# Kernel tuning notes

Hardware: AMD Instinct MI355X
Metric: run time of the kernel (lower is better)

The kernel has to match this reference:

```python
import jax, jax.numpy as jnp
import numpy as np

R_EARTH_KM = 6371.0

def haversine(lat1, lon1, lat2, lon2):
    # inputs in degrees, output distance in km
    lat1, lon1, lat2, lon2 = (jnp.radians(x) for x in (lat1, lon1, lat2, lon2))
    dlat = lat2 - lat1
    dlon = lon2 - lon1
    a = jnp.sin(dlat * 0.5) ** 2 + jnp.cos(lat1) * jnp.cos(lat2) * jnp.sin(dlon * 0.5) ** 2
    return 2.0 * R_EARTH_KM * jnp.arcsin(jnp.sqrt(jnp.clip(a, 0.0, 1.0)))

def _latlon(key, n):
    k1, k2 = jax.random.split(key)
    lat = jax.random.uniform(k1, (n,), minval=-90.0, maxval=90.0)
    lon = jax.random.uniform(k2, (n,), minval=-180.0, maxval=180.0)
    return jnp.stack([lat, lon], axis=1).astype(jnp.float32)

def setup_inputs() -> dict:
    key = jax.random.key(0)
    ks = jax.random.split(key, 12)
    B, D = 4096, 1792
    NC, NM, NF = 3000, 7000, 13000
    scale = 0.02
    return {
        'features': jax.random.normal(ks[0], (B, D), dtype=jnp.float32),
        'labels_2d': _latlon(ks[1], B),
        'coarse_partition': _latlon(ks[2], NC),
        'middle_partition': _latlon(ks[3], NM),
        'fine_partition': _latlon(ks[4], NF),
        'middle_parents': jax.random.randint(ks[5], (NM,), 0, NC, dtype=jnp.int32),
        'fine_parents': jax.random.randint(ks[6], (NF,), 0, NM, dtype=jnp.int32),
        'coarse_w': jax.random.normal(ks[7], (D, NC), dtype=jnp.float32) * scale,
        'coarse_b': jnp.zeros((NC,), dtype=jnp.float32),
        'middle_w': jax.random.normal(ks[8], (D, NM), dtype=jnp.float32) * scale,
        'middle_b': jnp.zeros((NM,), dtype=jnp.float32),
        'fine_w': jax.random.normal(ks[9], (D, NF), dtype=jnp.float32) * scale,
        'fine_b': jnp.zeros((NF,), dtype=jnp.float32),
    }

def _single_loss(labels_2d, logits, partition):
    # cartesian-product haversine cdist: [B, M]
    dists = haversine(labels_2d[:, 0:1], labels_2d[:, 1:2],
                      partition[None, :, 0], partition[None, :, 1])
    labels_index = jnp.argmin(dists, axis=1)
    logp = jax.nn.log_softmax(logits, axis=1)
    nll = -jnp.take_along_axis(logp, labels_index[:, None], axis=1)[:, 0]
    return jnp.mean(nll)

def reference(features, labels_2d, coarse_partition, middle_partition, fine_partition,
              middle_parents, fine_parents, coarse_w, coarse_b, middle_w, middle_b,
              fine_w, fine_b):
    coarse_logits = features @ coarse_w + coarse_b
    middle_logits = features @ middle_w + middle_b
    fine_logits = features @ fine_w + fine_b

    loss = (_single_loss(labels_2d, coarse_logits, coarse_partition)
            + _single_loss(labels_2d, middle_logits, middle_partition)
            + _single_loss(labels_2d, fine_logits, fine_partition))

    fine_probs = jax.nn.softmax(fine_logits, axis=1)
    middle_probs = jax.nn.softmax(middle_logits, axis=1)
    coarse_probs = jax.nn.softmax(coarse_logits, axis=1)
    # hierarchy combine: gather parent probs and multiply
    final_probs = (fine_probs
                   * middle_probs[:, fine_parents]
                   * coarse_probs[:, middle_parents[fine_parents]])

    predictions = fine_partition[jnp.argmax(final_probs, axis=1)]  # [B, 2]
    d = haversine(labels_2d[:, 0], labels_2d[:, 1], predictions[:, 0], predictions[:, 1])
    thresholds = jnp.array([1.0, 25.0, 200.0, 750.0, 2500.0], dtype=jnp.float32)
    acc = jnp.mean((d[None, :] <= thresholds[:, None]).astype(jnp.float32), axis=1)
    return loss, acc
```

## Files before the change

kernel.cpp:

```cpp
#include <hip/hip_runtime.h>
#include <hip/hip_fp16.h>
#include <math.h>

#define B_   4096
#define D_   1792
#define NC_  3000
#define NM_  7000
#define NF_  13000
#define NCP  3072
#define NMP  7040
#define NFP  13056
#define NTOT (NCP + NMP + NFP)
#define OFFC 0
#define OFFM NCP
#define OFFF (NCP + NMP)
#define FHALF 6528
#define WCHUNK 7040
#define DEG2RAD 0.017453292519943295f

typedef _Float16 half8  __attribute__((ext_vector_type(8)));
typedef _Float16 half4v __attribute__((ext_vector_type(4)));
typedef float    f32x4  __attribute__((ext_vector_type(4)));

__device__ __forceinline__ void async16(const void* g, void* l) {
  __builtin_amdgcn_global_load_lds(
      (const __attribute__((address_space(1))) void*)g,
      (__attribute__((address_space(3))) void*)l, 16, 0, 0);
}

__global__ void prep_kernel(const float* __restrict__ labels,
                            const float* __restrict__ cp, const float* __restrict__ mp,
                            const float* __restrict__ fp,
                            const float* __restrict__ cb, const float* __restrict__ mb,
                            const float* __restrict__ fb,
                            float* __restrict__ bias, float4* __restrict__ ptrig,
                            float4* __restrict__ ltrig, float* __restrict__ accum) {
  int i = blockIdx.x * 256 + threadIdx.x;
  if (i < NTOT) {
    float v = 0.f;
    if (i < OFFM)      { if (i < NC_) v = cb[i]; }
    else if (i < OFFF) { int j = i - OFFM; if (j < NM_) v = mb[j]; }
    else               { int j = i - OFFF; if (j < NF_) v = fb[j]; }
    bias[i] = v;
  }
  if (i < NC_ + NM_ + NF_) {
    const float* src; int j = i;
    if (i < NC_)            { src = cp; }
    else if (i < NC_ + NM_) { src = mp; j = i - NC_; }
    else                    { src = fp; j = i - NC_ - NM_; }
    float la = src[2 * j] * DEG2RAD, lo = src[2 * j + 1] * DEG2RAD;
    float sla, cla, slo, clo;
    sincosf(la, &sla, &cla); sincosf(lo, &slo, &clo);
    ptrig[i] = make_float4(sla, cla, slo, clo);
  }
  if (i < B_) {
    float la = labels[2 * i] * DEG2RAD, lo = labels[2 * i + 1] * DEG2RAD;
    float sla, cla, slo, clo;
    sincosf(la, &sla, &cla); sincosf(lo, &slo, &clo);
    ltrig[i] = make_float4(sla, cla, slo, clo);
  }
  if (i < 64) accum[i] = 0.f;
}

__global__ void cvt_feat(const float4* __restrict__ in, half4v* __restrict__ out) {
  int i = blockIdx.x * 256 + threadIdx.x;
  float4 v = in[i];
  half4v h;
  h[0] = (_Float16)v.x; h[1] = (_Float16)v.y; h[2] = (_Float16)v.z; h[3] = (_Float16)v.w;
  out[i] = h;
}

__global__ void transpose_w(const float* __restrict__ w, _Float16* __restrict__ wt,
                            int Nfull, int c0, int ntrue_chunk) {
  __shared__ float tile[32][33];
  int n0 = blockIdx.x * 32, k0 = blockIdx.y * 32;
  int tx = threadIdx.x, ty = threadIdx.y;
#pragma unroll
  for (int i = 0; i < 4; ++i) {
    int kk = ty + i * 8;
    int n = n0 + tx;
    float v = (n < ntrue_chunk) ? w[(size_t)(k0 + kk) * Nfull + c0 + n] : 0.f;
    tile[kk][tx] = v;
  }
  __syncthreads();
#pragma unroll
  for (int i = 0; i < 4; ++i) {
    int nn = ty + i * 8;
    wt[(size_t)(n0 + nn) * D_ + k0 + tx] = (_Float16)tile[tx][nn];
  }
}

__global__ void argmin_kernel(const float4* __restrict__ ptrig, const float4* __restrict__ ltrig,
                              int* __restrict__ lidx) {
  __shared__ float rv[256];
  __shared__ int ri[256];
  int b = blockIdx.x, tid = threadIdx.x;
  float4 lt = ltrig[b];
  const int base[3] = {0, NC_, NC_ + NM_};
  const int cnt[3]  = {NC_, NM_, NF_};
#pragma unroll
  for (int h = 0; h < 3; ++h) {
    float best = 1e30f; int bi = 0;
    for (int i = tid; i < cnt[h]; i += 256) {
      float4 pt = ptrig[base[h] + i];
      float cdla = lt.y * pt.y + lt.x * pt.x;
      float cdlo = lt.w * pt.w + lt.z * pt.z;
      float a = 0.5f * (1.f - cdla) + (lt.y * pt.y) * 0.5f * (1.f - cdlo);
      if (a < best) { best = a; bi = i; }
    }
    rv[tid] = best; ri[tid] = bi;
    __syncthreads();
    for (int o = 128; o; o >>= 1) {
      if (tid < o) {
        if (rv[tid + o] < rv[tid] || (rv[tid + o] == rv[tid] && ri[tid + o] < ri[tid])) {
          rv[tid] = rv[tid + o]; ri[tid] = ri[tid + o];
        }
      }
      __syncthreads();
    }
    if (tid == 0) lidx[h * B_ + b] = ri[0];
    __syncthreads();
  }
}

__global__ __launch_bounds__(256) void gemm_f16(const _Float16* __restrict__ A,
                                                const _Float16* __restrict__ Bt,
                                                const float* __restrict__ bias,
                                                _Float16* __restrict__ C, int coff) {
  __shared__ _Float16 tA[128 * 64];
  __shared__ _Float16 tB[128 * 64];
  const int tid = threadIdx.x;
  const int lane = tid & 63, w = tid >> 6;
  const int wm = w & 1, wn = w >> 1;
  const int q = lane >> 4, l15 = lane & 15;
  const int bx = blockIdx.x;
  const int mt = bx & 31, nt = bx >> 5;
  const int m0 = mt * 128;
  const int nl0 = nt * 128;
  const int gn0 = coff + nl0;

  f32x4 acc[4][4];
#pragma unroll
  for (int a = 0; a < 4; ++a)
#pragma unroll
    for (int b2 = 0; b2 < 4; ++b2) acc[a][b2] = (f32x4){0.f, 0.f, 0.f, 0.f};

  const int cbase = w * 256 + lane;
  int amoff[4], axor[4], bnoff[4], bxor[4];
#pragma unroll
  for (int t = 0; t < 4; ++t) {
    int ml = wm * 64 + t * 16 + l15;
    amoff[t] = ml * 64; axor[t] = ml & 7;
    int nl = wn * 64 + t * 16 + l15;
    bnoff[t] = nl * 64; bxor[t] = nl & 7;
  }

  for (int kt = 0; kt < 28; ++kt) {
    const int k0 = kt * 64;
#pragma unroll
    for (int t = 0; t < 4; ++t) {
      int c = cbase + t * 64;
      int m = c >> 3, slot = c & 7;
      int kb = slot ^ (m & 7);
      async16(A + (size_t)(m0 + m) * D_ + k0 + kb * 8, (void*)(tA + (w * 4 + t) * 512));
      async16(Bt + (size_t)(nl0 + m) * D_ + k0 + kb * 8, (void*)(tB + (w * 4 + t) * 512));
    }
    __syncthreads();
#pragma unroll
    for (int s = 0; s < 2; ++s) {
      half8 af[4], bf[4];
#pragma unroll
      for (int t = 0; t < 4; ++t) {
        af[t] = *(const half8*)(tA + amoff[t] + ((((s << 2) | q) ^ axor[t]) << 3));
        bf[t] = *(const half8*)(tB + bnoff[t] + ((((s << 2) | q) ^ bxor[t]) << 3));
      }
#pragma unroll
      for (int tm = 0; tm < 4; ++tm)
#pragma unroll
        for (int tn = 0; tn < 4; ++tn)
          acc[tm][tn] = __builtin_amdgcn_mfma_f32_16x16x32_f16(af[tm], bf[tn], acc[tm][tn], 0, 0, 0);
    }
    __syncthreads();
  }

  float bn[4];
#pragma unroll
  for (int tn = 0; tn < 4; ++tn) bn[tn] = bias[gn0 + wn * 64 + tn * 16 + l15];
#pragma unroll
  for (int tm = 0; tm < 4; ++tm) {
    int gm = m0 + wm * 64 + tm * 16 + q * 4;
#pragma unroll
    for (int tn = 0; tn < 4; ++tn) {
      int gn = gn0 + wn * 64 + tn * 16 + l15;
      _Float16* dst = C + (size_t)gm * NTOT + gn;
#pragma unroll
      for (int r = 0; r < 4; ++r) dst[(size_t)r * NTOT] = (_Float16)(acc[tm][tn][r] + bn[tn]);
    }
  }
}

__device__ __forceinline__ float block_lse(float m, float s, float* ms, float* ss, int tid) {
  ms[tid] = m; ss[tid] = s;
  __syncthreads();
  for (int o = 128; o; o >>= 1) {
    if (tid < o) {
      float m2 = ms[tid + o], s2 = ss[tid + o];
      if (m2 > ms[tid]) { ss[tid] = s2 + ss[tid] * __expf(ms[tid] - m2); ms[tid] = m2; }
      else ss[tid] += s2 * __expf(m2 - ms[tid]);
    }
    __syncthreads();
  }
  float r = ms[0] + logf(ss[0]);
  __syncthreads();
  return r;
}

__global__ __launch_bounds__(256) void final_kernel(const _Float16* __restrict__ logits,
                                                    const int* __restrict__ mpar,
                                                    const int* __restrict__ fpar,
                                                    const float4* __restrict__ ptrig,
                                                    const float4* __restrict__ ltrig,
                                                    const int* __restrict__ lidx,
                                                    float* __restrict__ nll_buf,
                                                    float* __restrict__ accum) {
  __shared__ float co[NC_];
  __shared__ float par[NM_];
  __shared__ float ms[256], ss[256];
  __shared__ int ri[256];
  int b = blockIdx.x, tid = threadIdx.x;
  const _Float16* row = logits + (size_t)b * NTOT;

  float m = -1e30f, s = 0.f;
  {
    const half8* rc = (const half8*)(row + OFFC);
    for (int i = tid; i < NC_ / 8; i += 256) {
      half8 v = rc[i];
      float x[8];
#pragma unroll
      for (int j = 0; j < 8; ++j) x[j] = (float)v[j];
      float vm = fmaxf(fmaxf(fmaxf(x[0], x[1]), fmaxf(x[2], x[3])),
                       fmaxf(fmaxf(x[4], x[5]), fmaxf(x[6], x[7])));
      if (vm > m) { s *= __expf(m - vm); m = vm; }
#pragma unroll
      for (int j = 0; j < 8; ++j) s += __expf(x[j] - m);
      f32x4 lo = {x[0], x[1], x[2], x[3]}, hi = {x[4], x[5], x[6], x[7]};
      *(f32x4*)(co + i * 8)     = lo;
      *(f32x4*)(co + i * 8 + 4) = hi;
    }
  }
  float lseC = block_lse(m, s, ms, ss, tid);

  m = -1e30f; s = 0.f;
  {
    const half8* rm = (const half8*)(row + OFFM);
    const int4* mp4 = (const int4*)mpar;
    for (int i = tid; i < NM_ / 8; i += 256) {
      half8 v = rm[i];
      int4 p0 = mp4[2 * i], p1 = mp4[2 * i + 1];
      float x[8];
#pragma unroll
      for (int j = 0; j < 8; ++j) x[j] = (float)v[j];
      float vm = fmaxf(fmaxf(fmaxf(x[0], x[1]), fmaxf(x[2], x[3])),
                       fmaxf(fmaxf(x[4], x[5]), fmaxf(x[6], x[7])));
      if (vm > m) { s *= __expf(m - vm); m = vm; }
#pragma unroll
      for (int j = 0; j < 8; ++j) s += __expf(x[j] - m);
      int pj[8] = {p0.x, p0.y, p0.z, p0.w, p1.x, p1.y, p1.z, p1.w};
      f32x4 lo = {x[0] + co[pj[0]], x[1] + co[pj[1]], x[2] + co[pj[2]], x[3] + co[pj[3]]};
      f32x4 hi = {x[4] + co[pj[4]], x[5] + co[pj[5]], x[6] + co[pj[6]], x[7] + co[pj[7]]};
      *(f32x4*)(par + i * 8)     = lo;
      *(f32x4*)(par + i * 8 + 4) = hi;
    }
  }
  float lseM = block_lse(m, s, ms, ss, tid);

  m = -1e30f; s = 0.f;
  float best = -1e30f; int bi = 0;
  {
    const half8* rf = (const half8*)(row + OFFF);
    const int4* fp4 = (const int4*)fpar;
    for (int i = tid; i < NF_ / 8; i += 256) {
      half8 v = rf[i];
      int4 p0 = fp4[2 * i], p1 = fp4[2 * i + 1];
      float x[8];
#pragma unroll
      for (int j = 0; j < 8; ++j) x[j] = (float)v[j];
      float vm = fmaxf(fmaxf(fmaxf(x[0], x[1]), fmaxf(x[2], x[3])),
                       fmaxf(fmaxf(x[4], x[5]), fmaxf(x[6], x[7])));
      if (vm > m) { s *= __expf(m - vm); m = vm; }
#pragma unroll
      for (int j = 0; j < 8; ++j) s += __expf(x[j] - m);
      int pj[8] = {p0.x, p0.y, p0.z, p0.w, p1.x, p1.y, p1.z, p1.w};
#pragma unroll
      for (int j = 0; j < 8; ++j) {
        float vv = x[j] + par[pj[j]];
        if (vv > best) { best = vv; bi = i * 8 + j; }
      }
    }
  }
  float lseF = block_lse(m, s, ms, ss, tid);

  ms[tid] = best; ri[tid] = bi;
  __syncthreads();
  for (int o = 128; o; o >>= 1) {
    if (tid < o) {
      if (ms[tid + o] > ms[tid] || (ms[tid + o] == ms[tid] && ri[tid + o] < ri[tid])) {
        ms[tid] = ms[tid + o]; ri[tid] = ri[tid + o];
      }
    }
    __syncthreads();
  }

  if (tid == 0) {
    int ic = lidx[b], im = lidx[B_ + b], ifn = lidx[2 * B_ + b];
    nll_buf[b] = (lseC - (float)row[OFFC + ic])
               + (lseM - (float)row[OFFM + im])
               + (lseF - (float)row[OFFF + ifn]);
    float4 pt = ptrig[NC_ + NM_ + ri[0]];
    float4 lt = ltrig[b];
    float cdla = lt.y * pt.y + lt.x * pt.x;
    float cdlo = lt.w * pt.w + lt.z * pt.z;
    float a = 0.5f * (1.f - cdla) + (lt.y * pt.y) * 0.5f * (1.f - cdlo);
    a = fminf(fmaxf(a, 0.f), 1.f);
    float d = 2.f * 6371.f * asinf(sqrtf(a));
    const float thr[5] = {1.f, 25.f, 200.f, 750.f, 2500.f};
#pragma unroll
    for (int j = 0; j < 5; ++j)
      if (d <= thr[j]) atomicAdd(accum + 1 + j, 1.f);
  }
}

__global__ void finish_kernel(const float* __restrict__ accum,
                              const float* __restrict__ nll, float* __restrict__ out) {
  __shared__ float sh[256];
  int tid = threadIdx.x;
  float s = 0.f;
  for (int i = tid; i < B_; i += 256) s += nll[i];
  sh[tid] = s;
  __syncthreads();
  for (int o = 128; o; o >>= 1) { if (tid < o) sh[tid] += sh[tid + o]; __syncthreads(); }
  if (tid == 0) out[0] = sh[0] * (1.f / 4096.f);
  if (tid >= 1 && tid < 6) out[tid] = accum[tid] * (1.f / 4096.f);
}

extern "C" void kernel_launch(void* const* d_in, const int* in_sizes, int n_in,
                              void* d_out, int out_size, void* d_ws, size_t ws_size,
                              hipStream_t stream) {
  (void)in_sizes; (void)n_in; (void)out_size; (void)ws_size;
  const float* features = (const float*)d_in[0];
  const float* labels   = (const float*)d_in[1];
  const float* cpart    = (const float*)d_in[2];
  const float* mpart    = (const float*)d_in[3];
  const float* fpart    = (const float*)d_in[4];
  const int*   mpar     = (const int*)d_in[5];
  const int*   fpar     = (const int*)d_in[6];
  const float* cw       = (const float*)d_in[7];
  const float* cb       = (const float*)d_in[8];
  const float* mw       = (const float*)d_in[9];
  const float* mb       = (const float*)d_in[10];
  const float* fw       = (const float*)d_in[11];
  const float* fb       = (const float*)d_in[12];
  float* out = (float*)d_out;

  char* ws = (char*)d_ws;
  size_t off = 0;
  auto alloc = [&](size_t bytes) {
    char* p = ws + off;
    off += (bytes + 255) & ~(size_t)255;
    return p;
  };
  _Float16* feat16 = (_Float16*)alloc((size_t)B_ * D_ * 2);
  _Float16* wTbuf  = (_Float16*)alloc((size_t)WCHUNK * D_ * 2);
  _Float16* logits = (_Float16*)alloc((size_t)B_ * NTOT * 2);
  float*    bias   = (float*)alloc((size_t)NTOT * 4);
  float4*   ptrig  = (float4*)alloc((size_t)(NC_ + NM_ + NF_) * 16);
  float4*   ltrig  = (float4*)alloc((size_t)B_ * 16);
  int*      lidx   = (int*)alloc((size_t)3 * B_ * 4);
  float*    nll    = (float*)alloc((size_t)B_ * 4);
  float*    accum  = (float*)alloc(64 * 4);

  prep_kernel<<<dim3(91), dim3(256), 0, stream>>>(labels, cpart, mpart, fpart, cb, mb, fb,
                                                  bias, ptrig, ltrig, accum);
  cvt_feat<<<dim3(B_ * D_ / 4 / 256), dim3(256), 0, stream>>>((const float4*)features,
                                                              (half4v*)feat16);
  argmin_kernel<<<dim3(B_), dim3(256), 0, stream>>>(ptrig, ltrig, lidx);

  transpose_w<<<dim3(NCP / 32, D_ / 32), dim3(32, 8), 0, stream>>>(cw, wTbuf, NC_, 0, NC_);
  gemm_f16<<<dim3(32 * (NCP / 128)), dim3(256), 0, stream>>>(feat16, wTbuf, bias, logits, OFFC);

  transpose_w<<<dim3(NMP / 32, D_ / 32), dim3(32, 8), 0, stream>>>(mw, wTbuf, NM_, 0, NM_);
  gemm_f16<<<dim3(32 * (NMP / 128)), dim3(256), 0, stream>>>(feat16, wTbuf, bias, logits, OFFM);

  transpose_w<<<dim3(FHALF / 32, D_ / 32), dim3(32, 8), 0, stream>>>(fw, wTbuf, NF_, 0, FHALF);
  gemm_f16<<<dim3(32 * (FHALF / 128)), dim3(256), 0, stream>>>(feat16, wTbuf, bias, logits, OFFF);

  transpose_w<<<dim3(FHALF / 32, D_ / 32), dim3(32, 8), 0, stream>>>(fw, wTbuf, NF_, FHALF, NF_ - FHALF);
  gemm_f16<<<dim3(32 * (FHALF / 128)), dim3(256), 0, stream>>>(feat16, wTbuf, bias, logits, OFFF + FHALF);

  final_kernel<<<dim3(B_), dim3(256), 0, stream>>>(logits, mpar, fpar, ptrig, ltrig,
                                                   lidx, nll, accum);
  finish_kernel<<<dim3(1), dim3(256), 0, stream>>>(accum, nll, out);
}
```

Before: 883.5 us.

## Rewrite GEMM with 256x256 tiles and multi-stage async LDS pipeline

Replaces the 128x128 single-buffered GEMM with a 512-thread 256x256 tile kernel. It uses a four-slot async global-to-LDS pipeline that splits K into 32-wide halves, plus explicit waitcnt/barrier scheduling and setprio around the MFMA bursts. The aim is to hide global load latency behind matrix work and raise arithmetic intensity per LDS byte. The partition sizes are padded to multiples of 256, which adds some wasted compute on padding columns and increases register pressure from the 8x4 accumulator array.

New measurement: 797.0 us. 1.11x faster.

```diff
diff --git a/kernel.cpp b/kernel.cpp
--- a/kernel.cpp
+++ b/kernel.cpp
@@ -8,14 +8,15 @@
 #define NM_  7000
 #define NF_  13000
 #define NCP  3072
-#define NMP  7040
-#define NFP  13056
+#define NMP  7168
+#define NFP  13312
 #define NTOT (NCP + NMP + NFP)
 #define OFFC 0
 #define OFFM NCP
 #define OFFF (NCP + NMP)
-#define FHALF 6528
-#define WCHUNK 7040
+#define FHALF 6656
+#define WCHUNK 7168
+#define NIT 14
 #define DEG2RAD 0.017453292519943295f
 
 typedef _Float16 half8  __attribute__((ext_vector_type(8)));
@@ -123,72 +124,129 @@
   }
 }
 
-__global__ __launch_bounds__(256) void gemm_f16(const _Float16* __restrict__ A,
-                                                const _Float16* __restrict__ Bt,
-                                                const float* __restrict__ bias,
-                                                _Float16* __restrict__ C, int coff) {
-  __shared__ _Float16 tA[128 * 64];
-  __shared__ _Float16 tB[128 * 64];
+#define LOADA(abase) { _Pragma("unroll") for (int tm = 0; tm < 8; ++tm) \
+    af[tm] = *(const half8*)(lds + (abase) + amB + tm * 512 + xsl); }
+#define LOADB(bbase, tn) (*(const half8*)(lds + (bbase) + bnB + (tn) * 512 + xsl))
+#define DO_MFMA(nh) { \
+    __builtin_amdgcn_s_setprio(1); \
+    _Pragma("unroll") for (int tm = 0; tm < 8; ++tm) { \
+      acc[tm][(nh)*2]   = __builtin_amdgcn_mfma_f32_16x16x32_f16(af[tm], b0, acc[tm][(nh)*2], 0,0,0); \
+      acc[tm][(nh)*2+1] = __builtin_amdgcn_mfma_f32_16x16x32_f16(af[tm], b1, acc[tm][(nh)*2+1], 0,0,0); \
+    } \
+    __builtin_amdgcn_s_setprio(0); }
+
+__global__ __launch_bounds__(512, 2) void gemm_f16(const _Float16* __restrict__ A,
+                                                   const _Float16* __restrict__ Bt,
+                                                   const float* __restrict__ bias,
+                                                   _Float16* __restrict__ C, int coff) {
+  __shared__ _Float16 lds[65536];
   const int tid = threadIdx.x;
   const int lane = tid & 63, w = tid >> 6;
   const int wm = w & 1, wn = w >> 1;
   const int q = lane >> 4, l15 = lane & 15;
   const int bx = blockIdx.x;
-  const int mt = bx & 31, nt = bx >> 5;
-  const int m0 = mt * 128;
-  const int nl0 = nt * 128;
+  const int mt = bx & 15, nt = bx >> 4;
+  const int m0 = mt * 256;
+  const int nl0 = nt * 256;
   const int gn0 = coff + nl0;
 
-  f32x4 acc[4][4];
-#pragma unroll
-  for (int a = 0; a < 4; ++a)
+  f32x4 acc[8][4];
+#pragma unroll
+  for (int a = 0; a < 8; ++a)
 #pragma unroll
     for (int b2 = 0; b2 < 4; ++b2) acc[a][b2] = (f32x4){0.f, 0.f, 0.f, 0.f};
 
-  const int cbase = w * 256 + lane;
-  int amoff[4], axor[4], bnoff[4], bxor[4];
-#pragma unroll
-  for (int t = 0; t < 4; ++t) {
-    int ml = wm * 64 + t * 16 + l15;
-    amoff[t] = ml * 64; axor[t] = ml & 7;
-    int nl = wn * 64 + t * 16 + l15;
-    bnoff[t] = nl * 64; bxor[t] = nl & 7;
-  }
-
-  for (int kt = 0; kt < 28; ++kt) {
-    const int k0 = kt * 64;
-#pragma unroll
-    for (int t = 0; t < 4; ++t) {
-      int c = cbase + t * 64;
-      int m = c >> 3, slot = c & 7;
-      int kb = slot ^ (m & 7);
-      async16(A + (size_t)(m0 + m) * D_ + k0 + kb * 8, (void*)(tA + (w * 4 + t) * 512));
-      async16(Bt + (size_t)(nl0 + m) * D_ + k0 + kb * 8, (void*)(tB + (w * 4 + t) * 512));
-    }
-    __syncthreads();
-#pragma unroll
-    for (int s = 0; s < 2; ++s) {
-      half8 af[4], bf[4];
-#pragma unroll
-      for (int t = 0; t < 4; ++t) {
-        af[t] = *(const half8*)(tA + amoff[t] + ((((s << 2) | q) ^ axor[t]) << 3));
-        bf[t] = *(const half8*)(tB + bnoff[t] + ((((s << 2) | q) ^ bxor[t]) << 3));
+  const int amB = (wm * 128 + l15) * 32;
+  const int bnB = (wn * 64 + l15) * 32;
+  const int xsl = ((q ^ ((l15 >> 1) & 3)) << 3);
+  const int kbl = (lane & 3) ^ ((lane >> 3) & 3);
+  const int rr = lane >> 2;
+
+  auto stage = [&](const _Float16* __restrict__ G, int row0, int ktile, int kh, int ldsoff) {
+    const int kk = ktile * 64 + (kh * 4 + kbl) * 8;
+#pragma unroll
+    for (int j = 0; j < 2; ++j) {
+      int seg = w * 2 + j;
+      async16(G + (size_t)(row0 + seg * 16 + rr) * D_ + kk,
+              (void*)(lds + ldsoff + seg * 512));
+    }
+  };
+
+  half8 af[8];
+
+  stage(A,  m0,  0, 0, 0);
+  stage(Bt, nl0, 0, 0, 32768);
+  stage(A,  m0,  0, 1, 8192);
+  stage(Bt, nl0, 0, 1, 40960);
+  stage(A,  m0,  1, 0, 16384);
+  stage(Bt, nl0, 1, 0, 49152);
+  asm volatile("s_waitcnt vmcnt(4)" ::: "memory");
+  __builtin_amdgcn_sched_barrier(0);
+  __builtin_amdgcn_s_barrier();
+
+#pragma unroll 1
+  for (int i = 0; i < NIT; ++i) {
+    const int t1 = 2 * i + 1, t2 = 2 * i + 2, t3 = 2 * i + 3;
+    const bool more = (i < NIT - 1);
+    LOADA(0);
+    { half8 b0 = LOADB(32768, 0), b1 = LOADB(32768, 1);
+      stage(A,  m0,  t1, 1, 24576);
+      stage(Bt, nl0, t1, 1, 57344);
+      __builtin_amdgcn_s_barrier();
+      DO_MFMA(0);
+      __builtin_amdgcn_s_barrier(); }
+    { half8 b0 = LOADB(32768, 2), b1 = LOADB(32768, 3);
+      __builtin_amdgcn_s_barrier();
+      DO_MFMA(1);
+      __builtin_amdgcn_s_barrier(); }
+    LOADA(8192);
+    { half8 b0 = LOADB(40960, 0), b1 = LOADB(40960, 1);
+      if (more) stage(A, m0, t2, 0, 0);
+      __builtin_amdgcn_s_barrier();
+      DO_MFMA(0);
+      __builtin_amdgcn_s_barrier(); }
+    { half8 b0 = LOADB(40960, 2), b1 = LOADB(40960, 3);
+      if (more) {
+        stage(Bt, nl0, t2, 0, 32768);
+        asm volatile("s_waitcnt vmcnt(4)" ::: "memory");
+      } else {
+        asm volatile("s_waitcnt vmcnt(0)" ::: "memory");
       }
-#pragma unroll
-      for (int tm = 0; tm < 4; ++tm)
-#pragma unroll
-        for (int tn = 0; tn < 4; ++tn)
-          acc[tm][tn] = __builtin_amdgcn_mfma_f32_16x16x32_f16(af[tm], bf[tn], acc[tm][tn], 0, 0, 0);
-    }
-    __syncthreads();
+      __builtin_amdgcn_sched_barrier(0);
+      __builtin_amdgcn_s_barrier();
+      DO_MFMA(1);
+      __builtin_amdgcn_s_barrier(); }
+    LOADA(16384);
+    { half8 b0 = LOADB(49152, 0), b1 = LOADB(49152, 1);
+      if (more) { stage(A, m0, t2, 1, 8192); stage(Bt, nl0, t2, 1, 40960); }
+      __builtin_amdgcn_s_barrier();
+      DO_MFMA(0);
+      __builtin_amdgcn_s_barrier(); }
+    { half8 b0 = LOADB(49152, 2), b1 = LOADB(49152, 3);
+      __builtin_amdgcn_s_barrier();
+      DO_MFMA(1);
+      __builtin_amdgcn_s_barrier(); }
+    LOADA(24576);
+    { half8 b0 = LOADB(57344, 0), b1 = LOADB(57344, 1);
+      if (more) stage(A, m0, t3, 0, 16384);
+      __builtin_amdgcn_s_barrier();
+      DO_MFMA(0);
+      __builtin_amdgcn_s_barrier(); }
+    { half8 b0 = LOADB(57344, 2), b1 = LOADB(57344, 3);
+      if (more) stage(Bt, nl0, t3, 0, 49152);
+      asm volatile("s_waitcnt vmcnt(4)" ::: "memory");
+      __builtin_amdgcn_sched_barrier(0);
+      __builtin_amdgcn_s_barrier();
+      DO_MFMA(1);
+      __builtin_amdgcn_s_barrier(); }
   }
 
   float bn[4];
 #pragma unroll
   for (int tn = 0; tn < 4; ++tn) bn[tn] = bias[gn0 + wn * 64 + tn * 16 + l15];
 #pragma unroll
-  for (int tm = 0; tm < 4; ++tm) {
-    int gm = m0 + wm * 64 + tm * 16 + q * 4;
+  for (int tm = 0; tm < 8; ++tm) {
+    int gm = m0 + wm * 128 + tm * 16 + q * 4;
 #pragma unroll
     for (int tn = 0; tn < 4; ++tn) {
       int gn = gn0 + wn * 64 + tn * 16 + l15;
@@ -379,23 +437,23 @@
   float*    nll    = (float*)alloc((size_t)B_ * 4);
   float*    accum  = (float*)alloc(64 * 4);
 
-  prep_kernel<<<dim3(91), dim3(256), 0, stream>>>(labels, cpart, mpart, fpart, cb, mb, fb,
-                                                  bias, ptrig, ltrig, accum);
+  prep_kernel<<<dim3(NTOT / 256), dim3(256), 0, stream>>>(labels, cpart, mpart, fpart,
+                                                          cb, mb, fb, bias, ptrig, ltrig, accum);
   cvt_feat<<<dim3(B_ * D_ / 4 / 256), dim3(256), 0, stream>>>((const float4*)features,
                                                               (half4v*)feat16);
   argmin_kernel<<<dim3(B_), dim3(256), 0, stream>>>(ptrig, ltrig, lidx);
 
   transpose_w<<<dim3(NCP / 32, D_ / 32), dim3(32, 8), 0, stream>>>(cw, wTbuf, NC_, 0, NC_);
-  gemm_f16<<<dim3(32 * (NCP / 128)), dim3(256), 0, stream>>>(feat16, wTbuf, bias, logits, OFFC);
+  gemm_f16<<<dim3(16 * (NCP / 256)), dim3(512), 0, stream>>>(feat16, wTbuf, bias, logits, OFFC);
 
   transpose_w<<<dim3(NMP / 32, D_ / 32), dim3(32, 8), 0, stream>>>(mw, wTbuf, NM_, 0, NM_);
-  gemm_f16<<<dim3(32 * (NMP / 128)), dim3(256), 0, stream>>>(feat16, wTbuf, bias, logits, OFFM);
+  gemm_f16<<<dim3(16 * (NMP / 256)), dim3(512), 0, stream>>>(feat16, wTbuf, bias, logits, OFFM);
 
   transpose_w<<<dim3(FHALF / 32, D_ / 32), dim3(32, 8), 0, stream>>>(fw, wTbuf, NF_, 0, FHALF);
-  gemm_f16<<<dim3(32 * (FHALF / 128)), dim3(256), 0, stream>>>(feat16, wTbuf, bias, logits, OFFF);
+  gemm_f16<<<dim3(16 * (FHALF / 256)), dim3(512), 0, stream>>>(feat16, wTbuf, bias, logits, OFFF);
 
   transpose_w<<<dim3(FHALF / 32, D_ / 32), dim3(32, 8), 0, stream>>>(fw, wTbuf, NF_, FHALF, NF_ - FHALF);
-  gemm_f16<<<dim3(32 * (FHALF / 128)), dim3(256), 0, stream>>>(feat16, wTbuf, bias, logits, OFFF + FHALF);
+  gemm_f16<<<dim3(16 * (FHALF / 256)), dim3(512), 0, stream>>>(feat16, wTbuf, bias, logits, OFFF + FHALF);
 
   final_kernel<<<dim3(B_), dim3(256), 0, stream>>>(logits, mpar, fpar, ptrig, ltrig,
                                                    lidx, nll, accum);
```
